# Performance work log

Hardware: AMD Instinct MI355X
Metric: run time of the kernel (lower is better)

Reference implementation:

```python
import jax, jax.numpy as jnp
import numpy as np

D_MODEL = 512      # hidden_dim
D_INNER = 1024     # 2 * hidden_dim (Mamba expand=2)
D_STATE = 16       # SSM state size N
DT_RANK = 32       # hidden_dim // 16
NBLK = 4           # num_blocks
KCONV = 4          # depthwise conv kernel
NHEAD = 4
NUM_LANES = 6
LANE_DIM = 128


def _rms(x, w, eps=1e-5):
    return x * jax.lax.rsqrt(jnp.mean(x * x, axis=-1, keepdims=True) + eps) * w


def _selective_scan(u, delta, A, Bm, Cm, Dv):
    # u, delta: [B,L,d]; A: [d,N]; Bm, Cm: [B,L,N]; Dv: [d]
    dA = jnp.exp(delta[..., None] * A)                 # [B,L,d,N]
    dBu = (delta * u)[..., None] * Bm[:, :, None, :]   # [B,L,d,N]

    def step(h, xs):
        dA_t, dBu_t = xs
        h = dA_t * h + dBu_t
        return h, h

    h0 = jnp.zeros(dA.shape[:1] + dA.shape[2:], dA.dtype)  # [B,d,N]
    _, hs = jax.lax.scan(step, h0, (jnp.swapaxes(dA, 0, 1), jnp.swapaxes(dBu, 0, 1)))
    y = jnp.einsum('lbdn,bln->bld', hs, Cm)            # [B,L,d]
    return y + u * Dv


def _mamba(lane_features, lane_in_W, lane_in_b, norm_w, in_proj_W, conv_w, conv_b,
           x_proj_W, dt_proj_W, dt_proj_b, A_log, D_skip, out_proj_W, final_norm_w):
    x = lane_features @ lane_in_W + lane_in_b          # [B,L,D_MODEL]
    for i in range(NBLK):
        h = _rms(x, norm_w[i])
        xz = h @ in_proj_W[i]                          # [B,L,2*D_INNER]
        xc, z = jnp.split(xz, 2, axis=-1)
        xt = jnp.swapaxes(xc, 1, 2)                    # [B,d,L]
        conv = jax.lax.conv_general_dilated(
            xt, conv_w[i][:, None, :], (1,), [(KCONV - 1, 0)],
            feature_group_count=D_INNER,
            dimension_numbers=('NCH', 'OIH', 'NCH')) + conv_b[i][:, None]
        xc = jax.nn.silu(jnp.swapaxes(conv, 1, 2))     # causal depthwise conv + SiLU
        dbl = xc @ x_proj_W[i]
        dt = dbl[..., :DT_RANK]
        Bm = dbl[..., DT_RANK:DT_RANK + D_STATE]
        Cm = dbl[..., DT_RANK + D_STATE:]
        delta = jax.nn.softplus(dt @ dt_proj_W[i] + dt_proj_b[i])
        y = _selective_scan(xc, delta, -jnp.exp(A_log[i]), Bm, Cm, D_skip[i])
        x = x + (y * jax.nn.silu(z)) @ out_proj_W[i]
    return _rms(x, final_norm_w)


def _mha(q_in, kv_in, Wq, bq, Wk, bk, Wv, bv, Wo, bo):
    B, Lq, _ = q_in.shape
    Lk = kv_in.shape[1]
    dh = D_MODEL // NHEAD
    q = (q_in @ Wq + bq).reshape(B, Lq, NHEAD, dh).transpose(0, 2, 1, 3)
    k = (kv_in @ Wk + bk).reshape(B, Lk, NHEAD, dh).transpose(0, 2, 1, 3)
    v = (kv_in @ Wv + bv).reshape(B, Lk, NHEAD, dh).transpose(0, 2, 1, 3)
    attn = jax.nn.softmax(jnp.einsum('bhqd,bhkd->bhqk', q, k) / np.sqrt(dh).astype(np.float32), axis=-1)
    o = jnp.einsum('bhqk,bhkd->bhqd', attn, v).transpose(0, 2, 1, 3).reshape(B, Lq, D_MODEL)
    return o @ Wo + bo


def setup_inputs() -> dict:
    key = jax.random.key(0)
    ks = iter(jax.random.split(key, 40))
    def n(shape, s=0.02):
        return jax.random.normal(next(ks), shape, jnp.float32) * s
    inp = {}
    inp['agent_features'] = jax.random.normal(next(ks), (8, 256, D_MODEL), jnp.float32)
    inp['lane_features'] = jax.random.normal(next(ks), (8, 512, LANE_DIM), jnp.float32)
    inp['lane_in_W'] = n((LANE_DIM, D_MODEL))
    inp['lane_in_b'] = jnp.zeros((D_MODEL,), jnp.float32)
    inp['norm_w'] = jnp.ones((NBLK, D_MODEL), jnp.float32)
    inp['in_proj_W'] = n((NBLK, D_MODEL, 2 * D_INNER))
    inp['conv_w'] = n((NBLK, D_INNER, KCONV), 0.2)
    inp['conv_b'] = jnp.zeros((NBLK, D_INNER), jnp.float32)
    inp['x_proj_W'] = n((NBLK, D_INNER, DT_RANK + 2 * D_STATE))
    inp['dt_proj_W'] = n((NBLK, DT_RANK, D_INNER), 0.1)
    inp['dt_proj_b'] = n((NBLK, D_INNER), 0.1)
    inp['A_log'] = jnp.tile(jnp.log(jnp.arange(1, D_STATE + 1, dtype=jnp.float32)), (NBLK, D_INNER, 1))
    inp['D_skip'] = jnp.ones((NBLK, D_INNER), jnp.float32)
    inp['out_proj_W'] = n((NBLK, D_INNER, D_MODEL))
    inp['final_norm_w'] = jnp.ones((D_MODEL,), jnp.float32)
    for name in ['Wq', 'Wk', 'Wv', 'Wo']:
        inp[name] = n((D_MODEL, D_MODEL))
    for name in ['bq', 'bk', 'bv', 'bo']:
        inp[name] = jnp.zeros((D_MODEL,), jnp.float32)
    inp['lin_in_W'] = n((D_MODEL, D_MODEL))
    inp['lin_in_b'] = jnp.zeros((D_MODEL,), jnp.float32)
    inp['lin_out_W'] = n((D_MODEL, NUM_LANES))
    inp['lin_out_b'] = jnp.zeros((NUM_LANES,), jnp.float32)
    return inp


def reference(agent_features, lane_features, lane_in_W, lane_in_b, norm_w, in_proj_W,
              conv_w, conv_b, x_proj_W, dt_proj_W, dt_proj_b, A_log, D_skip, out_proj_W,
              final_norm_w, Wq, Wk, Wv, Wo, bq, bk, bv, bo,
              lin_in_W, lin_in_b, lin_out_W, lin_out_b):
    enhanced = _mamba(lane_features, lane_in_W, lane_in_b, norm_w, in_proj_W, conv_w,
                      conv_b, x_proj_W, dt_proj_W, dt_proj_b, A_log, D_skip,
                      out_proj_W, final_norm_w)
    attn_out = _mha(enhanced, agent_features, Wq, bq, Wk, bk, Wv, bv, Wo, bo)
    probs = (attn_out @ lin_in_W + lin_in_b) @ lin_out_W + lin_out_b
    preds = jnp.argmax(probs, axis=-1)
    return probs, preds
```

## Files before the change

### kernel.cpp

```cpp
#include <hip/hip_runtime.h>
#include <math.h>

#define BATCH 8
#define LSEQ 512
#define LAGENT 256
#define DMODEL 512
#define DINNER 1024
#define DSTATE 16
#define DTRANK 32
#define NHEAD 4
#define DHEAD 128
#define NLANES 6

typedef __attribute__((ext_vector_type(8))) short bf16x8;
typedef __attribute__((ext_vector_type(4))) float f32x4;

__device__ __forceinline__ void split3(float x, short& h, short& m, short& l)
{
    unsigned hb = __float_as_uint(x) & 0xFFFF0000u;
    h = (short)(hb >> 16);
    float r1 = x - __uint_as_float(hb);
    unsigned mb = __float_as_uint(r1) & 0xFFFF0000u;
    m = (short)(mb >> 16);
    float r2 = r1 - __uint_as_float(mb);
    l = (short)(__float_as_uint(r2) >> 16);
}

__global__ __launch_bounds__(256)
void wsplit_k(const float* __restrict__ W, short* __restrict__ Wp, int K, int N)
{
    int gid = blockIdx.x * 256 + threadIdx.x;
    int lane = gid & 63;
    int rest = gid >> 6;
    int nsl = N >> 4;
    int ns = rest % nsl, kc = rest / nsl;
    int lrow = lane & 15, quad = lane >> 4;
    const float* src = W + (size_t)(kc * 32 + quad * 8) * N + ns * 16 + lrow;
    bf16x8 h, m, l;
#pragma unroll
    for (int j = 0; j < 8; ++j) {
        short hh, mm, ll;
        split3(src[(size_t)j * N], hh, mm, ll);
        h[j] = hh; m[j] = mm; l[j] = ll;
    }
    size_t planeS = (size_t)K * N;
    size_t base = ((size_t)(kc * nsl + ns)) * 512 + lane * 8;
    *(bf16x8*)&Wp[base] = h;
    *(bf16x8*)&Wp[planeS + base] = m;
    *(bf16x8*)&Wp[2 * planeS + base] = l;
}

template<int BM, int BN, int WM, int WN>
__global__ __launch_bounds__(256)
void gemm6(const float* __restrict__ A, int lda,
           const float* __restrict__ W,
           const float* __restrict__ bias,
           float* __restrict__ C, int ldc,
           int M, int N, int K, int act, int addC)
{
    constexpr int MT = BM / WM / 16;
    constexpr int NT = BN / WN / 16;
    constexpr int ASL = BM / 16;
    constexpr int BSL = BN / 16;
    __shared__ short Asl[3][ASL * 520];
    __shared__ short Bsl[3][BSL * 520];

    const int tid = threadIdx.x;
    const int w = tid >> 6, lane = tid & 63;
    const int lrow = lane & 15, quad = lane >> 4;
    const int aslab0 = (w % WM) * MT;
    const int bslab0 = (w / WM) * NT;
    const int m0 = blockIdx.y * BM, n0 = blockIdx.x * BN;

    f32x4 acc[MT][NT] = {};

    for (int k0 = 0; k0 < K; k0 += 32) {
        __syncthreads();
#pragma unroll
        for (int i = 0; i < BM / 32; ++i) {
            int v = tid + 256 * i;
            int row = v >> 3;
            int kq = (v & 7) * 4;
            float4 val = *(const float4*)&A[(size_t)(m0 + row) * lda + k0 + kq];
            int off = (row >> 4) * 520 + (((kq >> 3) << 4) + (row & 15)) * 8 + (kq & 7);
            short h[4], mm_[4], l[4];
            split3(val.x, h[0], mm_[0], l[0]);
            split3(val.y, h[1], mm_[1], l[1]);
            split3(val.z, h[2], mm_[2], l[2]);
            split3(val.w, h[3], mm_[3], l[3]);
            *(short4*)&Asl[0][off] = make_short4(h[0], h[1], h[2], h[3]);
            *(short4*)&Asl[1][off] = make_short4(mm_[0], mm_[1], mm_[2], mm_[3]);
            *(short4*)&Asl[2][off] = make_short4(l[0], l[1], l[2], l[3]);
        }
        constexpr int NPQS = (BN == 128) ? 5 : 4;
#pragma unroll
        for (int i = 0; i < BN / 64; ++i) {
            int v = tid + 256 * i;
            int kp = v >> NPQS;
            int nc = (v & ((1 << NPQS) - 1)) * 4;
            int k1 = kp * 2;
            float4 r0 = *(const float4*)&W[(size_t)(k0 + k1) * N + n0 + nc];
            float4 r1 = *(const float4*)&W[(size_t)(k0 + k1 + 1) * N + n0 + nc];
            const float e0[4] = {r0.x, r0.y, r0.z, r0.w};
            const float e1[4] = {r1.x, r1.y, r1.z, r1.w};
#pragma unroll
            for (int e = 0; e < 4; ++e) {
                int n = nc + e;
                int off = (n >> 4) * 520 + (((k1 >> 3) << 4) + (n & 15)) * 8 + (k1 & 7);
                short h0, m0_, l0, h1, m1_, l1;
                split3(e0[e], h0, m0_, l0);
                split3(e1[e], h1, m1_, l1);
                *(short2*)&Bsl[0][off] = make_short2(h0, h1);
                *(short2*)&Bsl[1][off] = make_short2(m0_, m1_);
                *(short2*)&Bsl[2][off] = make_short2(l0, l1);
            }
        }
        __syncthreads();

        bf16x8 af[3][MT];
#pragma unroll
        for (int p = 0; p < 3; ++p)
#pragma unroll
            for (int i = 0; i < MT; ++i)
                af[p][i] = *(const bf16x8*)&Asl[p][(aslab0 + i) * 520 + lane * 8];

#pragma unroll
        for (int pb = 0; pb < 3; ++pb) {
            bf16x8 bfr[NT];
#pragma unroll
            for (int j = 0; j < NT; ++j)
                bfr[j] = *(const bf16x8*)&Bsl[pb][(bslab0 + j) * 520 + lane * 8];
            const int npa = (pb == 0) ? 3 : (pb == 1 ? 2 : 1);
#pragma unroll
            for (int pa = 0; pa < 3; ++pa) {
                if (pa >= npa) break;
#pragma unroll
                for (int i = 0; i < MT; ++i)
#pragma unroll
                    for (int j = 0; j < NT; ++j)
                        acc[i][j] = __builtin_amdgcn_mfma_f32_16x16x32_bf16(
                            af[pa][i], bfr[j], acc[i][j], 0, 0, 0);
            }
        }
    }

#pragma unroll
    for (int i = 0; i < MT; ++i) {
        int mbase = m0 + (aslab0 + i) * 16 + quad * 4;
#pragma unroll
        for (int j = 0; j < NT; ++j) {
            int n = n0 + (bslab0 + j) * 16 + lrow;
            float bv = bias ? bias[n] : 0.f;
#pragma unroll
            for (int r = 0; r < 4; ++r) {
                size_t off = (size_t)(mbase + r) * ldc + n;
                float v = acc[i][j][r] + bv;
                if (act == 1) v = (v > 20.f) ? v : log1pf(__expf(v));
                if (addC) v += C[off];
                C[off] = v;
            }
        }
    }
}

template<int BM, int BN, int WM, int WN>
__global__ __launch_bounds__(256)
void gemm6f(const unsigned short* __restrict__ Ap0,
            const unsigned short* __restrict__ Ap1,
            const unsigned short* __restrict__ Ap2, int lda,
            const short* __restrict__ Wp,
            const float* __restrict__ bias,
            float* __restrict__ C, int ldc,
            int M, int N, int K, int act, int addC)
{
    constexpr int MT = BM / WM / 16;
    constexpr int NT = BN / WN / 16;
    constexpr int ASL = BM / 16;
    constexpr int BSL = BN / 16;
    constexpr int BITER = (3 * BSL) / 4;
    constexpr int PSH = (BSL == 8) ? 9 : 8;
    __shared__ short Asl[3][ASL * 520];
    __shared__ short Bsl[3][BSL * 512];

    const int tid = threadIdx.x;
    const int w = tid >> 6, lane = tid & 63;
    const int lrow = lane & 15, quad = lane >> 4;
    const int aslab0 = (w % WM) * MT;
    const int bslab0 = (w / WM) * NT;
    const int m0 = blockIdx.y * BM, n0 = blockIdx.x * BN;
    const size_t planeS = (size_t)K * N;

    f32x4 acc[MT][NT] = {};

    for (int k0 = 0; k0 < K; k0 += 32) {
        __syncthreads();
#pragma unroll
        for (int i = 0; i < BM / 32; ++i) {
            int v = tid + 256 * i;
            int row = v >> 3;
            int kq = (v & 7) * 4;
            size_t g = (size_t)(m0 + row) * lda + k0 + kq;
            int off = (row >> 4) * 520 + (((kq >> 3) << 4) + (row & 15)) * 8 + (kq & 7);
            *(short4*)&Asl[0][off] = *(const short4*)&Ap0[g];
            *(short4*)&Asl[1][off] = *(const short4*)&Ap1[g];
            *(short4*)&Asl[2][off] = *(const short4*)&Ap2[g];
        }
        {
            const short* wb = Wp + ((size_t)(k0 >> 5) * (N >> 4) + (n0 >> 4)) * 512;
#pragma unroll
            for (int i = 0; i < BITER; ++i) {
                int idx = tid + 256 * i;
                int p = idx >> PSH;
                int r = idx & ((1 << PSH) - 1);
                *(int4*)&Bsl[p][r * 8] = *(const int4*)(wb + p * planeS + r * 8);
            }
        }
        __syncthreads();

        bf16x8 af[3][MT];
#pragma unroll
        for (int p = 0; p < 3; ++p)
#pragma unroll
            for (int i = 0; i < MT; ++i)
                af[p][i] = *(const bf16x8*)&Asl[p][(aslab0 + i) * 520 + lane * 8];

#pragma unroll
        for (int pb = 0; pb < 3; ++pb) {
            bf16x8 bfr[NT];
#pragma unroll
            for (int j = 0; j < NT; ++j)
                bfr[j] = *(const bf16x8*)&Bsl[pb][(bslab0 + j) * 512 + lane * 8];
            const int npa = (pb == 0) ? 3 : (pb == 1 ? 2 : 1);
#pragma unroll
            for (int pa = 0; pa < 3; ++pa) {
                if (pa >= npa) break;
#pragma unroll
                for (int i = 0; i < MT; ++i)
#pragma unroll
                    for (int j = 0; j < NT; ++j)
                        acc[i][j] = __builtin_amdgcn_mfma_f32_16x16x32_bf16(
                            af[pa][i], bfr[j], acc[i][j], 0, 0, 0);
            }
        }
    }

#pragma unroll
    for (int i = 0; i < MT; ++i) {
        int mbase = m0 + (aslab0 + i) * 16 + quad * 4;
#pragma unroll
        for (int j = 0; j < NT; ++j) {
            int n = n0 + (bslab0 + j) * 16 + lrow;
            float bv = bias ? bias[n] : 0.f;
#pragma unroll
            for (int r = 0; r < 4; ++r) {
                size_t off = (size_t)(mbase + r) * ldc + n;
                float v = acc[i][j][r] + bv;
                if (act == 1) v = (v > 20.f) ? v : log1pf(__expf(v));
                if (addC) v += C[off];
                C[off] = v;
            }
        }
    }
}

template<int BM, int BN, int WM, int WN>
__global__ __launch_bounds__(256)
void gemm6g(const float* __restrict__ A, int lda,
            const short* __restrict__ Wp,
            const float* __restrict__ bias,
            float* __restrict__ C, int ldc,
            int M, int N, int K, int act, int addC)
{
    constexpr int MT = BM / WM / 16;
    constexpr int NT = BN / WN / 16;
    constexpr int ASL = BM / 16;
    constexpr int BSL = BN / 16;
    constexpr int BITER = (3 * BSL) / 4;
    constexpr int PSH = (BSL == 8) ? 9 : 8;
    __shared__ short Asl[3][ASL * 520];
    __shared__ short Bsl[3][BSL * 512];

    const int tid = threadIdx.x;
    const int w = tid >> 6, lane = tid & 63;
    const int lrow = lane & 15, quad = lane >> 4;
    const int aslab0 = (w % WM) * MT;
    const int bslab0 = (w / WM) * NT;
    const int m0 = blockIdx.y * BM, n0 = blockIdx.x * BN;
    const size_t planeS = (size_t)K * N;

    f32x4 acc[MT][NT] = {};

    for (int k0 = 0; k0 < K; k0 += 32) {
        __syncthreads();
#pragma unroll
        for (int i = 0; i < BM / 32; ++i) {
            int v = tid + 256 * i;
            int row = v >> 3;
            int kq = (v & 7) * 4;
            float4 val = *(const float4*)&A[(size_t)(m0 + row) * lda + k0 + kq];
            int off = (row >> 4) * 520 + (((kq >> 3) << 4) + (row & 15)) * 8 + (kq & 7);
            short h[4], mm_[4], l[4];
            split3(val.x, h[0], mm_[0], l[0]);
            split3(val.y, h[1], mm_[1], l[1]);
            split3(val.z, h[2], mm_[2], l[2]);
            split3(val.w, h[3], mm_[3], l[3]);
            *(short4*)&Asl[0][off] = make_short4(h[0], h[1], h[2], h[3]);
            *(short4*)&Asl[1][off] = make_short4(mm_[0], mm_[1], mm_[2], mm_[3]);
            *(short4*)&Asl[2][off] = make_short4(l[0], l[1], l[2], l[3]);
        }
        {
            const short* wb = Wp + ((size_t)(k0 >> 5) * (N >> 4) + (n0 >> 4)) * 512;
#pragma unroll
            for (int i = 0; i < BITER; ++i) {
                int idx = tid + 256 * i;
                int p = idx >> PSH;
                int r = idx & ((1 << PSH) - 1);
                *(int4*)&Bsl[p][r * 8] = *(const int4*)(wb + p * planeS + r * 8);
            }
        }
        __syncthreads();

        bf16x8 af[3][MT];
#pragma unroll
        for (int p = 0; p < 3; ++p)
#pragma unroll
            for (int i = 0; i < MT; ++i)
                af[p][i] = *(const bf16x8*)&Asl[p][(aslab0 + i) * 520 + lane * 8];

#pragma unroll
        for (int pb = 0; pb < 3; ++pb) {
            bf16x8 bfr[NT];
#pragma unroll
            for (int j = 0; j < NT; ++j)
                bfr[j] = *(const bf16x8*)&Bsl[pb][(bslab0 + j) * 512 + lane * 8];
            const int npa = (pb == 0) ? 3 : (pb == 1 ? 2 : 1);
#pragma unroll
            for (int pa = 0; pa < 3; ++pa) {
                if (pa >= npa) break;
#pragma unroll
                for (int i = 0; i < MT; ++i)
#pragma unroll
                    for (int j = 0; j < NT; ++j)
                        acc[i][j] = __builtin_amdgcn_mfma_f32_16x16x32_bf16(
                            af[pa][i], bfr[j], acc[i][j], 0, 0, 0);
            }
        }
    }

#pragma unroll
    for (int i = 0; i < MT; ++i) {
        int mbase = m0 + (aslab0 + i) * 16 + quad * 4;
#pragma unroll
        for (int j = 0; j < NT; ++j) {
            int n = n0 + (bslab0 + j) * 16 + lrow;
            float bv = bias ? bias[n] : 0.f;
#pragma unroll
            for (int r = 0; r < 4; ++r) {
                size_t off = (size_t)(mbase + r) * ldc + n;
                float v = acc[i][j][r] + bv;
                if (act == 1) v = (v > 20.f) ? v : log1pf(__expf(v));
                if (addC) v += C[off];
                C[off] = v;
            }
        }
    }
}

__global__ __launch_bounds__(256)
void gemm6sk(const float* __restrict__ A, int lda,
             const float* __restrict__ W, int N,
             float* __restrict__ P, int M, int KC)
{
    constexpr int BM = 64, BN = 64, WM = 2, WN = 2;
    constexpr int MT = BM / WM / 16, NT = BN / WN / 16;
    __shared__ short Asl[3][4 * 520];
    __shared__ short Bsl[3][4 * 520];

    const int tid = threadIdx.x;
    const int w = tid >> 6, lane = tid & 63;
    const int lrow = lane & 15, quad = lane >> 4;
    const int aslab0 = (w % WM) * MT;
    const int bslab0 = (w / WM) * NT;
    const int m0 = blockIdx.y * BM, n0 = blockIdx.x * BN;
    const int kbeg = blockIdx.z * KC;

    f32x4 acc[MT][NT] = {};

    for (int k0 = kbeg; k0 < kbeg + KC; k0 += 32) {
        __syncthreads();
#pragma unroll
        for (int i = 0; i < BM / 32; ++i) {
            int v = tid + 256 * i;
            int row = v >> 3;
            int kq = (v & 7) * 4;
            float4 val = *(const float4*)&A[(size_t)(m0 + row) * lda + k0 + kq];
            int off = (row >> 4) * 520 + (((kq >> 3) << 4) + (row & 15)) * 8 + (kq & 7);
            short h[4], mm_[4], l[4];
            split3(val.x, h[0], mm_[0], l[0]);
            split3(val.y, h[1], mm_[1], l[1]);
            split3(val.z, h[2], mm_[2], l[2]);
            split3(val.w, h[3], mm_[3], l[3]);
            *(short4*)&Asl[0][off] = make_short4(h[0], h[1], h[2], h[3]);
            *(short4*)&Asl[1][off] = make_short4(mm_[0], mm_[1], mm_[2], mm_[3]);
            *(short4*)&Asl[2][off] = make_short4(l[0], l[1], l[2], l[3]);
        }
        {
            int v = tid;
            int kp = v >> 4;
            int nc = (v & 15) * 4;
            int k1 = kp * 2;
            float4 r0 = *(const float4*)&W[(size_t)(k0 + k1) * N + n0 + nc];
            float4 r1 = *(const float4*)&W[(size_t)(k0 + k1 + 1) * N + n0 + nc];
            const float e0[4] = {r0.x, r0.y, r0.z, r0.w};
            const float e1[4] = {r1.x, r1.y, r1.z, r1.w};
#pragma unroll
            for (int e = 0; e < 4; ++e) {
                int n = nc + e;
                int off = (n >> 4) * 520 + (((k1 >> 3) << 4) + (n & 15)) * 8 + (k1 & 7);
                short h0, m0_, l0, h1, m1_, l1;
                split3(e0[e], h0, m0_, l0);
                split3(e1[e], h1, m1_, l1);
                *(short2*)&Bsl[0][off] = make_short2(h0, h1);
                *(short2*)&Bsl[1][off] = make_short2(m0_, m1_);
                *(short2*)&Bsl[2][off] = make_short2(l0, l1);
            }
        }
        __syncthreads();

        bf16x8 af[3][MT];
#pragma unroll
        for (int p = 0; p < 3; ++p)
#pragma unroll
            for (int i = 0; i < MT; ++i)
                af[p][i] = *(const bf16x8*)&Asl[p][(aslab0 + i) * 520 + lane * 8];

#pragma unroll
        for (int pb = 0; pb < 3; ++pb) {
            bf16x8 bfr[NT];
#pragma unroll
            for (int j = 0; j < NT; ++j)
                bfr[j] = *(const bf16x8*)&Bsl[pb][(bslab0 + j) * 520 + lane * 8];
            const int npa = (pb == 0) ? 3 : (pb == 1 ? 2 : 1);
#pragma unroll
            for (int pa = 0; pa < 3; ++pa) {
                if (pa >= npa) break;
#pragma unroll
                for (int i = 0; i < MT; ++i)
#pragma unroll
                    for (int j = 0; j < NT; ++j)
                        acc[i][j] = __builtin_amdgcn_mfma_f32_16x16x32_bf16(
                            af[pa][i], bfr[j], acc[i][j], 0, 0, 0);
            }
        }
    }

    float* Pz = P + (size_t)blockIdx.z * M * 64;
#pragma unroll
    for (int i = 0; i < MT; ++i) {
        int mbase = m0 + (aslab0 + i) * 16 + quad * 4;
// ... 34 lines not shown
#pragma unroll
    for (int j = 0; j < 8; ++j) { v[j] = xr[lane + 64 * j]; ss = fmaf(v[j], v[j], ss); }
#pragma unroll
    for (int off = 32; off >= 1; off >>= 1) ss += __shfl_xor(ss, off);
    float scale = rsqrtf(ss * (1.f / 512.f) + 1e-5f);
#pragma unroll
    for (int j = 0; j < 8; ++j) {
        int col = lane + 64 * j;
        float val = v[j] * scale * w[col];
        short hh, mm, ll;
        split3(val, hh, mm, ll);
        size_t o = (size_t)row * DMODEL + col;
        P0[o] = (unsigned short)hh;
        P1[o] = (unsigned short)mm;
        P2[o] = (unsigned short)ll;
    }
}

__global__ __launch_bounds__(256)
void conv_silu_k(const float* __restrict__ XZ, const float* __restrict__ cw,
                 const float* __restrict__ cb, float* __restrict__ XC)
{
    int idx = blockIdx.x * 256 + threadIdx.x;
    int d4 = (idx & 255) * 4;
    int t = (idx >> 8) & 511;
    int b = idx >> 17;
    float4 wv[4];
#pragma unroll
    for (int e = 0; e < 4; ++e) wv[e] = *(const float4*)&cw[(d4 + e) * 4];
    float4 bv = *(const float4*)&cb[d4];
    float s[4] = {bv.x, bv.y, bv.z, bv.w};
#pragma unroll
    for (int k = 0; k < 4; ++k) {
        int tt = t + k - 3;
        if (tt >= 0) {
            float4 x = *(const float4*)&XZ[((size_t)(b * 512 + tt)) * 2048 + d4];
            const float xe[4] = {x.x, x.y, x.z, x.w};
            const float we[4] = {wv[0][k], wv[1][k], wv[2][k], wv[3][k]};
#pragma unroll
            for (int e = 0; e < 4; ++e) s[e] = fmaf(we[e], xe[e], s[e]);
        }
    }
    float4 o;
    o.x = s[0] / (1.f + __expf(-s[0]));
    o.y = s[1] / (1.f + __expf(-s[1]));
    o.z = s[2] / (1.f + __expf(-s[2]));
    o.w = s[3] / (1.f + __expf(-s[3]));
    *(float4*)&XC[((size_t)(b * 512 + t)) * 1024 + d4] = o;
}

__global__ __launch_bounds__(128)
void scan1_k(const float* __restrict__ DELTA, const float* __restrict__ XC,
             const float* __restrict__ DBL, const float* __restrict__ A_log,
             const float* __restrict__ Dsk, float* __restrict__ Y,
             float* __restrict__ SC, float* __restrict__ DS)
{
    __shared__ float BC[64][32];
    const int tid = threadIdx.x;
    const int d = blockIdx.x * 128 + tid;
    const int chunk = blockIdx.y;
    const int b = blockIdx.z;
    const int t0 = chunk * 64;

#pragma unroll
    for (int i = 0; i < 16; ++i) {
        int idx = tid + 128 * i;
        int t = idx >> 5, j = idx & 31;
        BC[t][j] = DBL[(size_t)(b * 512 + t0 + t) * 64 + 32 + j];
    }
    float Ac[16];
#pragma unroll
    for (int n = 0; n < 16; ++n) Ac[n] = -__expf(A_log[d * 16 + n]);
    float Dv = Dsk[d];
    __syncthreads();

    const float* dp = DELTA + ((size_t)(b * 512 + t0)) * 1024 + d;
    const float* up = XC    + ((size_t)(b * 512 + t0)) * 1024 + d;
    float* yp       = Y     + ((size_t)(b * 512 + t0)) * 1024 + d;

    float h[16];
#pragma unroll
    for (int n = 0; n < 16; ++n) h[n] = 0.f;
    float dsum = 0.f;

#pragma unroll 2
    for (int t = 0; t < 64; ++t) {
        float delta = dp[t * 1024];
        float u = up[t * 1024];
        dsum += delta;
        float du = delta * u;
        float y = 0.f;
#pragma unroll
        for (int n = 0; n < 16; ++n) {
            h[n] = fmaf(__expf(delta * Ac[n]), h[n], du * BC[t][n]);
            y = fmaf(h[n], BC[t][16 + n], y);
        }
        yp[t * 1024] = fmaf(u, Dv, y);
    }

    float* sc = SC + ((size_t)((b * 8 + chunk) * 1024 + d)) * 16;
#pragma unroll
    for (int n = 0; n < 16; ++n) sc[n] = h[n];
    DS[(size_t)(b * 8 + chunk) * 1024 + d] = dsum;
}

__global__ __launch_bounds__(256)
void scan2_k(const float* __restrict__ A_log, float* __restrict__ SC,
             const float* __restrict__ DS)
{
    int gid = blockIdx.x * 256 + threadIdx.x;
    int n = gid & 15;
    int d = (gid >> 4) & 1023;
    int b = gid >> 14;
    float Ac = -__expf(A_log[d * 16 + n]);
    float carry = 0.f;
#pragma unroll
    for (int c = 0; c < 8; ++c) {
        size_t off = ((size_t)((b * 8 + c) * 1024 + d)) * 16 + n;
        float s = SC[off];
        SC[off] = carry;
        carry = fmaf(__expf(Ac * DS[(size_t)(b * 8 + c) * 1024 + d]), carry, s);
    }
}

__global__ __launch_bounds__(128)
void scan3_k(const float* __restrict__ DELTA, const float* __restrict__ DBL,
             const float* __restrict__ A_log, const float* __restrict__ H0,
             const float* __restrict__ XZ, float* __restrict__ Y)
{
    __shared__ float Cs[64][16];
    const int tid = threadIdx.x;
    const int d = blockIdx.x * 128 + tid;
    const int chunk = blockIdx.y;
    const int b = blockIdx.z;
    const int t0 = chunk * 64;

#pragma unroll
    for (int i = 0; i < 8; ++i) {
        int idx = tid + 128 * i;
        int t = idx >> 4, j = idx & 15;
        Cs[t][j] = DBL[(size_t)(b * 512 + t0 + t) * 64 + 48 + j];
    }
    float Ac[16], h0[16];
#pragma unroll
    for (int n = 0; n < 16; ++n) Ac[n] = -__expf(A_log[d * 16 + n]);
    const float* h0p = H0 + ((size_t)((b * 8 + chunk) * 1024 + d)) * 16;
#pragma unroll
    for (int n = 0; n < 16; ++n) h0[n] = h0p[n];
    __syncthreads();

    const float* dp = DELTA + ((size_t)(b * 512 + t0)) * 1024 + d;
    const float* zp = XZ    + ((size_t)(b * 512 + t0)) * 2048 + 1024 + d;
    float* yp       = Y     + ((size_t)(b * 512 + t0)) * 1024 + d;

    float cum = 0.f;
    if (chunk == 0) {
#pragma unroll 2
        for (int t = 0; t < 64; ++t) {
            float z = zp[t * 2048];
            yp[t * 1024] *= z / (1.f + __expf(-z));
        }
    } else {
#pragma unroll 2
        for (int t = 0; t < 64; ++t) {
            float delta = dp[t * 1024];
            cum += delta;
            float p = 0.f;
#pragma unroll
            for (int n = 0; n < 16; ++n)
                p = fmaf(h0[n] * __expf(Ac[n] * cum), Cs[t][n], p);
            float z = zp[t * 2048];
            float yv = yp[t * 1024] + p;
            yp[t * 1024] = yv * (z / (1.f + __expf(-z)));
        }
    }
}

__global__ __launch_bounds__(256, 1)
void attn_mfma(const float* __restrict__ Qm, const float* __restrict__ Km,
               const float* __restrict__ Vm, float* __restrict__ CTX)
{
    __shared__ short KVs[3][16 * 520];
    __shared__ float Ps[4][16 * 260];
    const int tid = threadIdx.x;
    const int w = tid >> 6, lane = tid & 63;
    const int lrow = lane & 15, quad = lane >> 4;
    const int b = blockIdx.z, h = blockIdx.y;
    const int qw = blockIdx.x * 64 + w * 16;

    bf16x8 qf[3][4];
    {
        const float* qp = Qm + ((size_t)(b * 512 + qw + lrow)) * 512 + h * 128 + quad * 8;
#pragma unroll
        for (int kb = 0; kb < 4; ++kb) {
            float4 v0 = *(const float4*)(qp + kb * 32);
            float4 v1 = *(const float4*)(qp + kb * 32 + 4);
            const float e[8] = {v0.x, v0.y, v0.z, v0.w, v1.x, v1.y, v1.z, v1.w};
#pragma unroll
            for (int j = 0; j < 8; ++j) {
                short hh, mm, ll;
                split3(e[j], hh, mm, ll);
                qf[0][kb][j] = hh; qf[1][kb][j] = mm; qf[2][kb][j] = ll;
            }
        }
    }

    const int sdd = (tid & 31) * 4;
    const int skvb = tid >> 5;
    f32x4 sa[4][4] = {};

    float4 kpre[8];
#pragma unroll
    for (int i = 0; i < 8; ++i)
        kpre[i] = *(const float4*)&Km[((size_t)(b * 256 + skvb + 8 * i)) * 512 + h * 128 + sdd];

    for (int c = 0; c < 4; ++c) {
        if (c) __syncthreads();
        {
            const int kb = sdd >> 5, qd = (sdd >> 3) & 3, jd = sdd & 7;
#pragma unroll
            for (int i = 0; i < 8; ++i) {
                int kv = skvb + 8 * i;
                int off = ((kv >> 4) * 4 + kb) * 520 + ((kv & 15) + 16 * qd) * 8 + jd;
                short h0,m0,l0,h1,m1,l1,h2,m2,l2,h3,m3,l3;
                split3(kpre[i].x,h0,m0,l0); split3(kpre[i].y,h1,m1,l1);
                split3(kpre[i].z,h2,m2,l2); split3(kpre[i].w,h3,m3,l3);
// ... 188 lines not shown
            if (v > best) { best = v; bi = c; }
        }
        out[(size_t)4096 * 6 + row] = (float)bi;
    }
}

extern "C" void kernel_launch(void* const* d_in, const int* in_sizes, int n_in,
                              void* d_out, int out_size, void* d_ws, size_t ws_size,
                              hipStream_t stream)
{
    (void)in_sizes; (void)n_in; (void)out_size; (void)ws_size;
    const float* agent      = (const float*)d_in[0];
    const float* lane       = (const float*)d_in[1];
    const float* lane_in_W  = (const float*)d_in[2];
    const float* lane_in_b  = (const float*)d_in[3];
    const float* norm_w     = (const float*)d_in[4];
    const float* in_proj_W  = (const float*)d_in[5];
    const float* conv_w     = (const float*)d_in[6];
    const float* conv_b     = (const float*)d_in[7];
    const float* x_proj_W   = (const float*)d_in[8];
    const float* dt_proj_W  = (const float*)d_in[9];
    const float* dt_proj_b  = (const float*)d_in[10];
    const float* A_log      = (const float*)d_in[11];
    const float* D_skip     = (const float*)d_in[12];
    const float* out_proj_W = (const float*)d_in[13];
    const float* final_norm_w = (const float*)d_in[14];
    const float* Wq = (const float*)d_in[15];
    const float* Wk = (const float*)d_in[16];
    const float* Wv = (const float*)d_in[17];
    const float* Wo = (const float*)d_in[18];
    const float* bq = (const float*)d_in[19];
    const float* bk = (const float*)d_in[20];
    const float* bv = (const float*)d_in[21];
    const float* bo = (const float*)d_in[22];
    const float* lin_in_W  = (const float*)d_in[23];
    const float* lin_in_b  = (const float*)d_in[24];
    const float* lin_out_W = (const float*)d_in[25];
    const float* lin_out_b = (const float*)d_in[26];

    float* ws = (float*)d_ws;
    float* X     = ws;
    float* H     = X + (1 << 21);
    float* XZ    = H + (1 << 21);
    float* XC    = XZ + (1 << 23);
    float* DELTA = XC + (1 << 22);
    float* Y     = DELTA + (1 << 22);
    float* DBL   = Y + (1 << 22);
    unsigned short* Hp0 = (unsigned short*)H;
    unsigned short* Hp1 = (unsigned short*)(H + (1 << 20));
    unsigned short* Hp2 = (unsigned short*)Y;
    float* PART  = Y + (1 << 20);
    float* SCb   = H;
    float* DSb   = H + (1 << 20);
    short* WPL   = (short*)XC;
    float* Qb  = XZ;
    float* Kb  = XZ + (1 << 21);
    float* Vb  = Kb + (1 << 20);
    float* CTX = Vb + (1 << 20);
    float* AO  = CTX + (1 << 21);
    float* T2  = DELTA;

    dim3 blk(256);
    dim3 sblk(128);
    dim3 sgrid(8, 8, 8);

    wsplit_k<<<32, blk, 0, stream>>>(lane_in_W, WPL, 128, 512);
    gemm6g<128, 64, 2, 2><<<dim3(8, 32), blk, 0, stream>>>(
        lane, 128, WPL, lane_in_b, X, 512, 4096, 512, 128, 0, 0);

    for (int i = 0; i < 4; ++i) {
        rmsnorm3_k<<<1024, blk, 0, stream>>>(X, norm_w + i * 512, Hp0, Hp1, Hp2);
        wsplit_k<<<512, blk, 0, stream>>>(in_proj_W + (size_t)i * 512 * 2048, WPL, 512, 2048);
        gemm6f<128, 128, 2, 2><<<dim3(16, 32), blk, 0, stream>>>(
            Hp0, Hp1, Hp2, 512, WPL, nullptr, XZ, 2048, 4096, 2048, 512, 0, 0);
        conv_silu_k<<<4096, blk, 0, stream>>>(XZ, conv_w + i * 4096, conv_b + i * 1024, XC);
        gemm6sk<<<dim3(1, 64, 8), blk, 0, stream>>>(
            XC, 1024, x_proj_W + (size_t)i * 1024 * 64, 64, PART, 4096, 128);
        xred_k<<<256, blk, 0, stream>>>(PART, DBL);
        gemm6<128, 64, 2, 2><<<dim3(16, 32), blk, 0, stream>>>(
            DBL, 64, dt_proj_W + (size_t)i * 32 * 1024, dt_proj_b + i * 1024,
            DELTA, 1024, 4096, 1024, 32, 1, 0);
        scan1_k<<<sgrid, sblk, 0, stream>>>(DELTA, XC, DBL, A_log + (size_t)i * 1024 * 16,
                                            D_skip + i * 1024, Y, SCb, DSb);
        scan2_k<<<512, blk, 0, stream>>>(A_log + (size_t)i * 1024 * 16, SCb, DSb);
        wsplit_k<<<256, blk, 0, stream>>>(out_proj_W + (size_t)i * 1024 * 512, WPL, 1024, 512);
        scan3_k<<<sgrid, sblk, 0, stream>>>(DELTA, DBL, A_log + (size_t)i * 1024 * 16,
                                            SCb, XZ, Y);
        gemm6g<64, 64, 2, 2><<<dim3(8, 64), blk, 0, stream>>>(
            Y, 1024, WPL, nullptr, X, 512, 4096, 512, 1024, 0, 1);
    }

    rmsnorm3_k<<<1024, blk, 0, stream>>>(X, final_norm_w, Hp0, Hp1, Hp2);

    short* WPq = WPL;
    short* WPk = WPL + 786432;
    short* WPv = WPL + 2 * 786432;
    short* WPo = WPL + 3 * 786432;
    short* WPn = WPL + 4 * 786432;
    wsplit_k<<<128, blk, 0, stream>>>(Wq, WPq, 512, 512);
    wsplit_k<<<128, blk, 0, stream>>>(Wk, WPk, 512, 512);
    wsplit_k<<<128, blk, 0, stream>>>(Wv, WPv, 512, 512);
    wsplit_k<<<128, blk, 0, stream>>>(Wo, WPo, 512, 512);
    wsplit_k<<<128, blk, 0, stream>>>(lin_in_W, WPn, 512, 512);

    gemm6f<128, 64, 2, 2><<<dim3(8, 32), blk, 0, stream>>>(
        Hp0, Hp1, Hp2, 512, WPq, bq, Qb, 512, 4096, 512, 512, 0, 0);
    gemm6g<64, 64, 2, 2><<<dim3(8, 32), blk, 0, stream>>>(
        agent, 512, WPk, bk, Kb, 512, 2048, 512, 512, 0, 0);
    gemm6g<64, 64, 2, 2><<<dim3(8, 32), blk, 0, stream>>>(
        agent, 512, WPv, bv, Vb, 512, 2048, 512, 512, 0, 0);
    attn_mfma<<<dim3(8, 4, 8), blk, 0, stream>>>(Qb, Kb, Vb, CTX);
    gemm6g<64, 64, 2, 2><<<dim3(8, 64), blk, 0, stream>>>(
        CTX, 512, WPo, bo, AO, 512, 4096, 512, 512, 0, 0);
    gemm6g<64, 64, 2, 2><<<dim3(8, 64), blk, 0, stream>>>(
        AO, 512, WPn, lin_in_b, T2, 512, 4096, 512, 512, 0, 0);
    head_k<<<1024, blk, 0, stream>>>(T2, lin_out_W, lin_out_b, (float*)d_out);
}
```

Measured before the change: 1.297 ms.

## Emit pre-split bf16 planes from scan3, pre-split dt_proj weights, batch weight splits

scan3 now applies the SiLU(z) gate and writes the three bf16 split planes directly, so the out_proj GEMM uses the pre-split-input path instead of splitting the fp32 activation per tile. scan1 writes its partial outputs into the free x half of the XZ buffer, and both scans batch their global loads four timesteps at a time. The dt_proj weights are pre-split with wsplit_k so the generic gemm6 kernel can be removed, and the five attention/head weight splits are merged into one launch. This adds more buffer aliasing to reason about and extra 16-bit scattered stores in scan3.

```diff
diff --git a/kernel.cpp b/kernel.cpp
--- a/kernel.cpp
+++ b/kernel.cpp
@@ -50,20 +50,54 @@
     *(bf16x8*)&Wp[2 * planeS + base] = l;
 }
 
+__global__ __launch_bounds__(256)
+void wsplit5_k(const float* __restrict__ W0, const float* __restrict__ W1,
+               const float* __restrict__ W2, const float* __restrict__ W3,
+               const float* __restrict__ W4, short* __restrict__ Wp)
+{
+    const float* Ws[5] = {W0, W1, W2, W3, W4};
+    const float* W = Ws[blockIdx.y];
+    short* dst = Wp + (size_t)blockIdx.y * 786432;
+    const int K = 512, N = 512;
+    int gid = blockIdx.x * 256 + threadIdx.x;
+    int lane = gid & 63;
+    int rest = gid >> 6;
+    int nsl = N >> 4;
+    int ns = rest % nsl, kc = rest / nsl;
+    int lrow = lane & 15, quad = lane >> 4;
+    const float* src = W + (size_t)(kc * 32 + quad * 8) * N + ns * 16 + lrow;
+    bf16x8 h, m, l;
+#pragma unroll
+    for (int j = 0; j < 8; ++j) {
+        short hh, mm, ll;
+        split3(src[(size_t)j * N], hh, mm, ll);
+        h[j] = hh; m[j] = mm; l[j] = ll;
+    }
+    size_t planeS = (size_t)K * N;
+    size_t base = ((size_t)(kc * nsl + ns)) * 512 + lane * 8;
+    *(bf16x8*)&dst[base] = h;
+    *(bf16x8*)&dst[planeS + base] = m;
+    *(bf16x8*)&dst[2 * planeS + base] = l;
+}
+
 template<int BM, int BN, int WM, int WN>
 __global__ __launch_bounds__(256)
-void gemm6(const float* __restrict__ A, int lda,
-           const float* __restrict__ W,
-           const float* __restrict__ bias,
-           float* __restrict__ C, int ldc,
-           int M, int N, int K, int act, int addC)
+void gemm6f(const unsigned short* __restrict__ Ap0,
+            const unsigned short* __restrict__ Ap1,
+            const unsigned short* __restrict__ Ap2, int lda,
+            const short* __restrict__ Wp,
+            const float* __restrict__ bias,
+            float* __restrict__ C, int ldc,
+            int M, int N, int K, int act, int addC)
 {
     constexpr int MT = BM / WM / 16;
     constexpr int NT = BN / WN / 16;
     constexpr int ASL = BM / 16;
     constexpr int BSL = BN / 16;
+    constexpr int BITER = (3 * BSL) / 4;
+    constexpr int PSH = (BSL == 8) ? 9 : 8;
     __shared__ short Asl[3][ASL * 520];
-    __shared__ short Bsl[3][BSL * 520];
+    __shared__ short Bsl[3][BSL * 512];
 
     const int tid = threadIdx.x;
     const int w = tid >> 6, lane = tid & 63;
@@ -71,6 +105,105 @@
     const int aslab0 = (w % WM) * MT;
     const int bslab0 = (w / WM) * NT;
     const int m0 = blockIdx.y * BM, n0 = blockIdx.x * BN;
+    const size_t planeS = (size_t)K * N;
+
+    f32x4 acc[MT][NT] = {};
+
+    for (int k0 = 0; k0 < K; k0 += 32) {
+        __syncthreads();
+#pragma unroll
+        for (int i = 0; i < BM / 32; ++i) {
+            int v = tid + 256 * i;
+            int row = v >> 3;
+            int kq = (v & 7) * 4;
+            size_t g = (size_t)(m0 + row) * lda + k0 + kq;
+            int off = (row >> 4) * 520 + (((kq >> 3) << 4) + (row & 15)) * 8 + (kq & 7);
+            *(short4*)&Asl[0][off] = *(const short4*)&Ap0[g];
+            *(short4*)&Asl[1][off] = *(const short4*)&Ap1[g];
+            *(short4*)&Asl[2][off] = *(const short4*)&Ap2[g];
+        }
+        {
+            const short* wb = Wp + ((size_t)(k0 >> 5) * (N >> 4) + (n0 >> 4)) * 512;
+#pragma unroll
+            for (int i = 0; i < BITER; ++i) {
+                int idx = tid + 256 * i;
+                int p = idx >> PSH;
+                int r = idx & ((1 << PSH) - 1);
+                *(int4*)&Bsl[p][r * 8] = *(const int4*)(wb + p * planeS + r * 8);
+            }
+        }
+        __syncthreads();
+
+        bf16x8 af[3][MT];
+#pragma unroll
+        for (int p = 0; p < 3; ++p)
+#pragma unroll
+            for (int i = 0; i < MT; ++i)
+                af[p][i] = *(const bf16x8*)&Asl[p][(aslab0 + i) * 520 + lane * 8];
+
+#pragma unroll
+        for (int pb = 0; pb < 3; ++pb) {
+            bf16x8 bfr[NT];
+#pragma unroll
+            for (int j = 0; j < NT; ++j)
+                bfr[j] = *(const bf16x8*)&Bsl[pb][(bslab0 + j) * 512 + lane * 8];
+            const int npa = (pb == 0) ? 3 : (pb == 1 ? 2 : 1);
+#pragma unroll
+            for (int pa = 0; pa < 3; ++pa) {
+                if (pa >= npa) break;
+#pragma unroll
+                for (int i = 0; i < MT; ++i)
+#pragma unroll
+                    for (int j = 0; j < NT; ++j)
+                        acc[i][j] = __builtin_amdgcn_mfma_f32_16x16x32_bf16(
+                            af[pa][i], bfr[j], acc[i][j], 0, 0, 0);
+            }
+        }
+    }
+
+#pragma unroll
+    for (int i = 0; i < MT; ++i) {
+        int mbase = m0 + (aslab0 + i) * 16 + quad * 4;
+#pragma unroll
+        for (int j = 0; j < NT; ++j) {
+            int n = n0 + (bslab0 + j) * 16 + lrow;
+            float bv = bias ? bias[n] : 0.f;
+#pragma unroll
+            for (int r = 0; r < 4; ++r) {
+                size_t off = (size_t)(mbase + r) * ldc + n;
+                float v = acc[i][j][r] + bv;
+                if (act == 1) v = (v > 20.f) ? v : log1pf(__expf(v));
+                if (addC) v += C[off];
+                C[off] = v;
+            }
+        }
+    }
+}
+
+template<int BM, int BN, int WM, int WN>
+__global__ __launch_bounds__(256)
+void gemm6g(const float* __restrict__ A, int lda,
+            const short* __restrict__ Wp,
+            const float* __restrict__ bias,
+            float* __restrict__ C, int ldc,
+            int M, int N, int K, int act, int addC)
+{
+    constexpr int MT = BM / WM / 16;
+    constexpr int NT = BN / WN / 16;
+    constexpr int ASL = BM / 16;
+    constexpr int BSL = BN / 16;
+    constexpr int BITER = (3 * BSL) / 4;
+    constexpr int PSH = (BSL == 8) ? 9 : 8;
+    __shared__ short Asl[3][ASL * 520];
+    __shared__ short Bsl[3][BSL * 512];
+
+    const int tid = threadIdx.x;
+    const int w = tid >> 6, lane = tid & 63;
+    const int lrow = lane & 15, quad = lane >> 4;
+    const int aslab0 = (w % WM) * MT;
+    const int bslab0 = (w / WM) * NT;
+    const int m0 = blockIdx.y * BM, n0 = blockIdx.x * BN;
+    const size_t planeS = (size_t)K * N;
 
     f32x4 acc[MT][NT] = {};
 
@@ -92,27 +225,14 @@
             *(short4*)&Asl[1][off] = make_short4(mm_[0], mm_[1], mm_[2], mm_[3]);
             *(short4*)&Asl[2][off] = make_short4(l[0], l[1], l[2], l[3]);
         }
-        constexpr int NPQS = (BN == 128) ? 5 : 4;
-#pragma unroll
-        for (int i = 0; i < BN / 64; ++i) {
-            int v = tid + 256 * i;
-            int kp = v >> NPQS;
-            int nc = (v & ((1 << NPQS) - 1)) * 4;
-            int k1 = kp * 2;
-            float4 r0 = *(const float4*)&W[(size_t)(k0 + k1) * N + n0 + nc];
-            float4 r1 = *(const float4*)&W[(size_t)(k0 + k1 + 1) * N + n0 + nc];
-            const float e0[4] = {r0.x, r0.y, r0.z, r0.w};
-            const float e1[4] = {r1.x, r1.y, r1.z, r1.w};
-#pragma unroll
-            for (int e = 0; e < 4; ++e) {
-                int n = nc + e;
-                int off = (n >> 4) * 520 + (((k1 >> 3) << 4) + (n & 15)) * 8 + (k1 & 7);
-                short h0, m0_, l0, h1, m1_, l1;
-                split3(e0[e], h0, m0_, l0);
-                split3(e1[e], h1, m1_, l1);
-                *(short2*)&Bsl[0][off] = make_short2(h0, h1);
-                *(short2*)&Bsl[1][off] = make_short2(m0_, m1_);
-                *(short2*)&Bsl[2][off] = make_short2(l0, l1);
+        {
+            const short* wb = Wp + ((size_t)(k0 >> 5) * (N >> 4) + (n0 >> 4)) * 512;
+#pragma unroll
+            for (int i = 0; i < BITER; ++i) {
+                int idx = tid + 256 * i;
+                int p = idx >> PSH;
+                int r = idx & ((1 << PSH) - 1);
+                *(int4*)&Bsl[p][r * 8] = *(const int4*)(wb + p * planeS + r * 8);
             }
         }
         __syncthreads();
@@ -129,7 +249,7 @@
             bf16x8 bfr[NT];
 #pragma unroll
             for (int j = 0; j < NT; ++j)
-                bfr[j] = *(const bf16x8*)&Bsl[pb][(bslab0 + j) * 520 + lane * 8];
+                bfr[j] = *(const bf16x8*)&Bsl[pb][(bslab0 + j) * 512 + lane * 8];
             const int npa = (pb == 0) ? 3 : (pb == 1 ? 2 : 1);
 #pragma unroll
             for (int pa = 0; pa < 3; ++pa) {
@@ -163,24 +283,15 @@
     }
 }
 
-template<int BM, int BN, int WM, int WN>
 __global__ __launch_bounds__(256)
-void gemm6f(const unsigned short* __restrict__ Ap0,
-            const unsigned short* __restrict__ Ap1,
-            const unsigned short* __restrict__ Ap2, int lda,
-            const short* __restrict__ Wp,
-            const float* __restrict__ bias,
-            float* __restrict__ C, int ldc,
-            int M, int N, int K, int act, int addC)
-{
-    constexpr int MT = BM / WM / 16;
-    constexpr int NT = BN / WN / 16;
-    constexpr int ASL = BM / 16;
-    constexpr int BSL = BN / 16;
-    constexpr int BITER = (3 * BSL) / 4;
-    constexpr int PSH = (BSL == 8) ? 9 : 8;
-    __shared__ short Asl[3][ASL * 520];
-    __shared__ short Bsl[3][BSL * 512];
+void gemm6sk(const float* __restrict__ A, int lda,
+             const float* __restrict__ W, int N,
+             float* __restrict__ P, int M, int KC)
+{
+    constexpr int BM = 64, BN = 64, WM = 2, WN = 2;
+    constexpr int MT = BM / WM / 16, NT = BN / WN / 16;
+    __shared__ short Asl[3][4 * 520];
+    __shared__ short Bsl[3][4 * 520];
 
     const int tid = threadIdx.x;
     const int w = tid >> 6, lane = tid & 63;
@@ -188,109 +299,11 @@
     const int aslab0 = (w % WM) * MT;
     const int bslab0 = (w / WM) * NT;
     const int m0 = blockIdx.y * BM, n0 = blockIdx.x * BN;
-    const size_t planeS = (size_t)K * N;
+    const int kbeg = blockIdx.z * KC;
 
     f32x4 acc[MT][NT] = {};
 
-    for (int k0 = 0; k0 < K; k0 += 32) {
-        __syncthreads();
-#pragma unroll
-        for (int i = 0; i < BM / 32; ++i) {
-            int v = tid + 256 * i;
-            int row = v >> 3;
-            int kq = (v & 7) * 4;
-            size_t g = (size_t)(m0 + row) * lda + k0 + kq;
-            int off = (row >> 4) * 520 + (((kq >> 3) << 4) + (row & 15)) * 8 + (kq & 7);
-            *(short4*)&Asl[0][off] = *(const short4*)&Ap0[g];
-            *(short4*)&Asl[1][off] = *(const short4*)&Ap1[g];
-            *(short4*)&Asl[2][off] = *(const short4*)&Ap2[g];
-        }
-        {
-            const short* wb = Wp + ((size_t)(k0 >> 5) * (N >> 4) + (n0 >> 4)) * 512;
-#pragma unroll
-            for (int i = 0; i < BITER; ++i) {
-                int idx = tid + 256 * i;
-                int p = idx >> PSH;
-                int r = idx & ((1 << PSH) - 1);
-                *(int4*)&Bsl[p][r * 8] = *(const int4*)(wb + p * planeS + r * 8);
-            }
-        }
-        __syncthreads();
-
-        bf16x8 af[3][MT];
-#pragma unroll
-        for (int p = 0; p < 3; ++p)
-#pragma unroll
-            for (int i = 0; i < MT; ++i)
-                af[p][i] = *(const bf16x8*)&Asl[p][(aslab0 + i) * 520 + lane * 8];
-
-#pragma unroll
-        for (int pb = 0; pb < 3; ++pb) {
-            bf16x8 bfr[NT];
-#pragma unroll
-            for (int j = 0; j < NT; ++j)
-                bfr[j] = *(const bf16x8*)&Bsl[pb][(bslab0 + j) * 512 + lane * 8];
-            const int npa = (pb == 0) ? 3 : (pb == 1 ? 2 : 1);
-#pragma unroll
-            for (int pa = 0; pa < 3; ++pa) {
-                if (pa >= npa) break;
-#pragma unroll
-                for (int i = 0; i < MT; ++i)
-#pragma unroll
-                    for (int j = 0; j < NT; ++j)
-                        acc[i][j] = __builtin_amdgcn_mfma_f32_16x16x32_bf16(
-                            af[pa][i], bfr[j], acc[i][j], 0, 0, 0);
-            }
-        }
-    }
-
-#pragma unroll
-    for (int i = 0; i < MT; ++i) {
-        int mbase = m0 + (aslab0 + i) * 16 + quad * 4;
-#pragma unroll
-        for (int j = 0; j < NT; ++j) {
-            int n = n0 + (bslab0 + j) * 16 + lrow;
-            float bv = bias ? bias[n] : 0.f;
-#pragma unroll
-            for (int r = 0; r < 4; ++r) {
-                size_t off = (size_t)(mbase + r) * ldc + n;
-                float v = acc[i][j][r] + bv;
-                if (act == 1) v = (v > 20.f) ? v : log1pf(__expf(v));
-                if (addC) v += C[off];
-                C[off] = v;
-            }
-        }
-    }
-}
-
-template<int BM, int BN, int WM, int WN>
-__global__ __launch_bounds__(256)
-void gemm6g(const float* __restrict__ A, int lda,
-            const short* __restrict__ Wp,
-            const float* __restrict__ bias,
-            float* __restrict__ C, int ldc,
-            int M, int N, int K, int act, int addC)
-{
-    constexpr int MT = BM / WM / 16;
-    constexpr int NT = BN / WN / 16;
-    constexpr int ASL = BM / 16;
-    constexpr int BSL = BN / 16;
-    constexpr int BITER = (3 * BSL) / 4;
-    constexpr int PSH = (BSL == 8) ? 9 : 8;
-    __shared__ short Asl[3][ASL * 520];
-    __shared__ short Bsl[3][BSL * 512];
-
-    const int tid = threadIdx.x;
-    const int w = tid >> 6, lane = tid & 63;
-    const int lrow = lane & 15, quad = lane >> 4;
-    const int aslab0 = (w % WM) * MT;
-    const int bslab0 = (w / WM) * NT;
-    const int m0 = blockIdx.y * BM, n0 = blockIdx.x * BN;
-    const size_t planeS = (size_t)K * N;
-
-    f32x4 acc[MT][NT] = {};
-
-    for (int k0 = 0; k0 < K; k0 += 32) {
+    for (int k0 = kbeg; k0 < kbeg + KC; k0 += 32) {
         __syncthreads();
 #pragma unroll
         for (int i = 0; i < BM / 32; ++i) {
@@ -309,102 +322,6 @@
             *(short4*)&Asl[2][off] = make_short4(l[0], l[1], l[2], l[3]);
         }
         {
-            const short* wb = Wp + ((size_t)(k0 >> 5) * (N >> 4) + (n0 >> 4)) * 512;
-#pragma unroll
-            for (int i = 0; i < BITER; ++i) {
-                int idx = tid + 256 * i;
-                int p = idx >> PSH;
-                int r = idx & ((1 << PSH) - 1);
-                *(int4*)&Bsl[p][r * 8] = *(const int4*)(wb + p * planeS + r * 8);
-            }
-        }
-        __syncthreads();
-
-        bf16x8 af[3][MT];
-#pragma unroll
-        for (int p = 0; p < 3; ++p)
-#pragma unroll
-            for (int i = 0; i < MT; ++i)
-                af[p][i] = *(const bf16x8*)&Asl[p][(aslab0 + i) * 520 + lane * 8];
-
-#pragma unroll
-        for (int pb = 0; pb < 3; ++pb) {
-            bf16x8 bfr[NT];
-#pragma unroll
-            for (int j = 0; j < NT; ++j)
-                bfr[j] = *(const bf16x8*)&Bsl[pb][(bslab0 + j) * 512 + lane * 8];
-            const int npa = (pb == 0) ? 3 : (pb == 1 ? 2 : 1);
-#pragma unroll
-            for (int pa = 0; pa < 3; ++pa) {
-                if (pa >= npa) break;
-#pragma unroll
-                for (int i = 0; i < MT; ++i)
-#pragma unroll
-                    for (int j = 0; j < NT; ++j)
-                        acc[i][j] = __builtin_amdgcn_mfma_f32_16x16x32_bf16(
-                            af[pa][i], bfr[j], acc[i][j], 0, 0, 0);
-            }
-        }
-    }
-
-#pragma unroll
-    for (int i = 0; i < MT; ++i) {
-        int mbase = m0 + (aslab0 + i) * 16 + quad * 4;
-#pragma unroll
-        for (int j = 0; j < NT; ++j) {
-            int n = n0 + (bslab0 + j) * 16 + lrow;
-            float bv = bias ? bias[n] : 0.f;
-#pragma unroll
-            for (int r = 0; r < 4; ++r) {
-                size_t off = (size_t)(mbase + r) * ldc + n;
-                float v = acc[i][j][r] + bv;
-                if (act == 1) v = (v > 20.f) ? v : log1pf(__expf(v));
-                if (addC) v += C[off];
-                C[off] = v;
-            }
-        }
-    }
-}
-
-__global__ __launch_bounds__(256)
-void gemm6sk(const float* __restrict__ A, int lda,
-             const float* __restrict__ W, int N,
-             float* __restrict__ P, int M, int KC)
-{
-    constexpr int BM = 64, BN = 64, WM = 2, WN = 2;
-    constexpr int MT = BM / WM / 16, NT = BN / WN / 16;
-    __shared__ short Asl[3][4 * 520];
-    __shared__ short Bsl[3][4 * 520];
-
-    const int tid = threadIdx.x;
-    const int w = tid >> 6, lane = tid & 63;
-    const int lrow = lane & 15, quad = lane >> 4;
-    const int aslab0 = (w % WM) * MT;
-    const int bslab0 = (w / WM) * NT;
-    const int m0 = blockIdx.y * BM, n0 = blockIdx.x * BN;
-    const int kbeg = blockIdx.z * KC;
-
-    f32x4 acc[MT][NT] = {};
-
-    for (int k0 = kbeg; k0 < kbeg + KC; k0 += 32) {
-        __syncthreads();
-#pragma unroll
-        for (int i = 0; i < BM / 32; ++i) {
-            int v = tid + 256 * i;
-            int row = v >> 3;
-            int kq = (v & 7) * 4;
-            float4 val = *(const float4*)&A[(size_t)(m0 + row) * lda + k0 + kq];
-            int off = (row >> 4) * 520 + (((kq >> 3) << 4) + (row & 15)) * 8 + (kq & 7);
-            short h[4], mm_[4], l[4];
-            split3(val.x, h[0], mm_[0], l[0]);
-            split3(val.y, h[1], mm_[1], l[1]);
-            split3(val.z, h[2], mm_[2], l[2]);
-            split3(val.w, h[3], mm_[3], l[3]);
-            *(short4*)&Asl[0][off] = make_short4(h[0], h[1], h[2], h[3]);
-            *(short4*)&Asl[1][off] = make_short4(mm_[0], mm_[1], mm_[2], mm_[3]);
-            *(short4*)&Asl[2][off] = make_short4(l[0], l[1], l[2], l[3]);
-        }
-        {
             int v = tid;
             int kp = v >> 4;
             int nc = (v & 15) * 4;
@@ -545,7 +462,7 @@
 __global__ __launch_bounds__(128)
 void scan1_k(const float* __restrict__ DELTA, const float* __restrict__ XC,
              const float* __restrict__ DBL, const float* __restrict__ A_log,
-             const float* __restrict__ Dsk, float* __restrict__ Y,
+             const float* __restrict__ Dsk, float* __restrict__ YL,
              float* __restrict__ SC, float* __restrict__ DS)
 {
     __shared__ float BC[64][32];
@@ -569,26 +486,34 @@
 
     const float* dp = DELTA + ((size_t)(b * 512 + t0)) * 1024 + d;
     const float* up = XC    + ((size_t)(b * 512 + t0)) * 1024 + d;
-    float* yp       = Y     + ((size_t)(b * 512 + t0)) * 1024 + d;
+    float* yp       = YL    + ((size_t)(b * 512 + t0)) * 2048 + d;
 
     float h[16];
 #pragma unroll
     for (int n = 0; n < 16; ++n) h[n] = 0.f;
     float dsum = 0.f;
 
-#pragma unroll 2
-    for (int t = 0; t < 64; ++t) {
-        float delta = dp[t * 1024];
-        float u = up[t * 1024];
-        dsum += delta;
-        float du = delta * u;
-        float y = 0.f;
-#pragma unroll
-        for (int n = 0; n < 16; ++n) {
-            h[n] = fmaf(__expf(delta * Ac[n]), h[n], du * BC[t][n]);
-            y = fmaf(h[n], BC[t][16 + n], y);
-        }
-        yp[t * 1024] = fmaf(u, Dv, y);
+    for (int tb = 0; tb < 64; tb += 4) {
+        float dl[4], ul[4];
+#pragma unroll
+        for (int j = 0; j < 4; ++j) {
+            dl[j] = dp[(tb + j) * 1024];
+            ul[j] = up[(tb + j) * 1024];
+        }
+#pragma unroll
+        for (int j = 0; j < 4; ++j) {
+            int t = tb + j;
+            float delta = dl[j], u = ul[j];
+            dsum += delta;
+            float du = delta * u;
+            float y = 0.f;
+#pragma unroll
+            for (int n = 0; n < 16; ++n) {
+                h[n] = fmaf(__expf(delta * Ac[n]), h[n], du * BC[t][n]);
+                y = fmaf(h[n], BC[t][16 + n], y);
+            }
+            yp[t * 2048] = fmaf(u, Dv, y);
+        }
     }
 
     float* sc = SC + ((size_t)((b * 8 + chunk) * 1024 + d)) * 16;
@@ -619,7 +544,8 @@
 __global__ __launch_bounds__(128)
 void scan3_k(const float* __restrict__ DELTA, const float* __restrict__ DBL,
              const float* __restrict__ A_log, const float* __restrict__ H0,
-             const float* __restrict__ XZ, float* __restrict__ Y)
+             const float* __restrict__ XZ, unsigned short* __restrict__ Yp0,
+             unsigned short* __restrict__ Yp1, unsigned short* __restrict__ Yp2)
 {
     __shared__ float Cs[64][16];
     const int tid = threadIdx.x;
@@ -643,28 +569,37 @@
     __syncthreads();
 
     const float* dp = DELTA + ((size_t)(b * 512 + t0)) * 1024 + d;
+    const float* yl = XZ    + ((size_t)(b * 512 + t0)) * 2048 + d;
     const float* zp = XZ    + ((size_t)(b * 512 + t0)) * 2048 + 1024 + d;
-    float* yp       = Y     + ((size_t)(b * 512 + t0)) * 1024 + d;
+    size_t obase = (size_t)(b * 512 + t0) * 1024 + d;
 
     float cum = 0.f;
-    if (chunk == 0) {
-#pragma unroll 2
-        for (int t = 0; t < 64; ++t) {
-            float z = zp[t * 2048];
-            yp[t * 1024] *= z / (1.f + __expf(-z));
-        }
-    } else {
-#pragma unroll 2
-        for (int t = 0; t < 64; ++t) {
-            float delta = dp[t * 1024];
-            cum += delta;
+    for (int tb = 0; tb < 64; tb += 4) {
+        float dl[4], yv[4], zl[4];
+#pragma unroll
+        for (int j = 0; j < 4; ++j) {
+            dl[j] = dp[(tb + j) * 1024];
+            yv[j] = yl[(tb + j) * 2048];
+            zl[j] = zp[(tb + j) * 2048];
+        }
+#pragma unroll
+        for (int j = 0; j < 4; ++j) {
+            int t = tb + j;
             float p = 0.f;
-#pragma unroll
-            for (int n = 0; n < 16; ++n)
-                p = fmaf(h0[n] * __expf(Ac[n] * cum), Cs[t][n], p);
-            float z = zp[t * 2048];
-            float yv = yp[t * 1024] + p;
-            yp[t * 1024] = yv * (z / (1.f + __expf(-z)));
+            if (chunk != 0) {
+                cum += dl[j];
+#pragma unroll
+                for (int n = 0; n < 16; ++n)
+                    p = fmaf(h0[n] * __expf(Ac[n] * cum), Cs[t][n], p);
+            }
+            float z = zl[j];
+            float g = (yv[j] + p) * (z / (1.f + __expf(-z)));
+            short hh, mm, ll;
+            split3(g, hh, mm, ll);
+            size_t o = obase + (size_t)t * 1024;
+            Yp0[o] = (unsigned short)hh;
+            Yp1[o] = (unsigned short)mm;
+            Yp2[o] = (unsigned short)ll;
         }
     }
 }
@@ -959,7 +894,11 @@
     float* PART  = Y + (1 << 20);
     float* SCb   = H;
     float* DSb   = H + (1 << 20);
+    short* DTWP  = (short*)(H + 3 * (1 << 19));
     short* WPL   = (short*)XC;
+    unsigned short* Yp0 = (unsigned short*)Y;
+    unsigned short* Yp1 = (unsigned short*)(Y + (1 << 21));
+    unsigned short* Yp2 = (unsigned short*)(XC + (1 << 20));
     float* Qb  = XZ;
     float* Kb  = XZ + (1 << 21);
     float* Vb  = Kb + (1 << 20);
@@ -984,17 +923,17 @@
         gemm6sk<<<dim3(1, 64, 8), blk, 0, stream>>>(
             XC, 1024, x_proj_W + (size_t)i * 1024 * 64, 64, PART, 4096, 128);
         xred_k<<<256, blk, 0, stream>>>(PART, DBL);
-        gemm6<128, 64, 2, 2><<<dim3(16, 32), blk, 0, stream>>>(
-            DBL, 64, dt_proj_W + (size_t)i * 32 * 1024, dt_proj_b + i * 1024,
-            DELTA, 1024, 4096, 1024, 32, 1, 0);
+        wsplit_k<<<16, blk, 0, stream>>>(dt_proj_W + (size_t)i * 32 * 1024, DTWP, 32, 1024);
+        gemm6g<128, 64, 2, 2><<<dim3(16, 32), blk, 0, stream>>>(
+            DBL, 64, DTWP, dt_proj_b + i * 1024, DELTA, 1024, 4096, 1024, 32, 1, 0);
         scan1_k<<<sgrid, sblk, 0, stream>>>(DELTA, XC, DBL, A_log + (size_t)i * 1024 * 16,
-                                            D_skip + i * 1024, Y, SCb, DSb);
+                                            D_skip + i * 1024, XZ, SCb, DSb);
         scan2_k<<<512, blk, 0, stream>>>(A_log + (size_t)i * 1024 * 16, SCb, DSb);
         wsplit_k<<<256, blk, 0, stream>>>(out_proj_W + (size_t)i * 1024 * 512, WPL, 1024, 512);
         scan3_k<<<sgrid, sblk, 0, stream>>>(DELTA, DBL, A_log + (size_t)i * 1024 * 16,
-                                            SCb, XZ, Y);
-        gemm6g<64, 64, 2, 2><<<dim3(8, 64), blk, 0, stream>>>(
-            Y, 1024, WPL, nullptr, X, 512, 4096, 512, 1024, 0, 1);
+                                            SCb, XZ, Yp0, Yp1, Yp2);
+        gemm6f<64, 64, 2, 2><<<dim3(8, 64), blk, 0, stream>>>(
+            Yp0, Yp1, Yp2, 1024, WPL, nullptr, X, 512, 4096, 512, 1024, 0, 1);
     }
 
     rmsnorm3_k<<<1024, blk, 0, stream>>>(X, final_norm_w, Hp0, Hp1, Hp2);
@@ -1004,11 +943,7 @@
     short* WPv = WPL + 2 * 786432;
     short* WPo = WPL + 3 * 786432;
     short* WPn = WPL + 4 * 786432;
-    wsplit_k<<<128, blk, 0, stream>>>(Wq, WPq, 512, 512);
-    wsplit_k<<<128, blk, 0, stream>>>(Wk, WPk, 512, 512);
-    wsplit_k<<<128, blk, 0, stream>>>(Wv, WPv, 512, 512);
-    wsplit_k<<<128, blk, 0, stream>>>(Wo, WPo, 512, 512);
-    wsplit_k<<<128, blk, 0, stream>>>(lin_in_W, WPn, 512, 512);
+    wsplit5_k<<<dim3(128, 5), blk, 0, stream>>>(Wq, Wk, Wv, Wo, lin_in_W, WPL);
 
     gemm6f<128, 64, 2, 2><<<dim3(8, 32), blk, 0, stream>>>(
         Hp0, Hp1, Hp2, 512, WPq, bq, Qb, 512, 4096, 512, 512, 0, 0);
```

Measured after the change: 1.437 ms. 1.11x slower.
